# Kernel tuning notes

Measured on AMD Instinct MI355X. Metric: run time of the kernel, lower is better.

Reference implementation:

```python
import jax, jax.numpy as jnp
import numpy as np

H, NH, NKV, HD, S, B = 4096, 32, 8, 128, 2048, 1
QMAX = 127.0  # int8 symmetric


def fake_quant(x, axis=None):
    """Symmetric int8 fake quantization with straight-through estimator.
    axis=None -> per-tensor dynamic scale; axis=int -> per-channel along that axis."""
    if axis is None:
        amax = jnp.max(jnp.abs(x))
    else:
        amax = jnp.max(jnp.abs(x), axis=axis, keepdims=True)
    scale = jnp.maximum(amax, 1e-8) / QMAX
    q = jnp.clip(jnp.round(x / scale), -QMAX - 1, QMAX) * scale
    return x + jax.lax.stop_gradient(q - x)


def quant_linear(x, w):
    # weight: per-output-channel quant (reduce over in-features axis=1);
    # activation: per-tensor dynamic quant
    xq = fake_quant(x)
    wq = fake_quant(w, axis=1)
    return jnp.einsum('bsh,oh->bso', xq, wq)


def rotate_half(x):
    x1, x2 = jnp.split(x, 2, axis=-1)
    return jnp.concatenate([-x2, x1], axis=-1)


def apply_rope(q, k, cos, sin):
    # q: [B,NH,S,HD], k: [B,NKV,S,HD], cos/sin: [B,S,HD]
    cos = cos[:, None, :, :]
    sin = sin[:, None, :, :]
    return q * cos + rotate_half(q) * sin, k * cos + rotate_half(k) * sin


def setup_inputs() -> dict:
    key = jax.random.key(0)
    ks = jax.random.split(key, 6)
    hidden_states = jax.random.normal(ks[0], (B, S, H), jnp.float32)
    # additive causal mask
    neg = jnp.finfo(jnp.float32).min
    mask = jnp.where(jnp.tril(jnp.ones((S, S), bool)), 0.0, neg)
    attention_mask = jnp.broadcast_to(mask, (B, 1, S, S)).astype(jnp.float32)
    # rotary cos/sin
    inv_freq = 1.0 / (10000.0 ** (jnp.arange(0, HD, 2, dtype=jnp.float32) / HD))
    t = jnp.arange(S, dtype=jnp.float32)
    freqs = jnp.outer(t, inv_freq)                     # [S, HD/2]
    emb = jnp.concatenate([freqs, freqs], axis=-1)     # [S, HD]
    cos = jnp.broadcast_to(jnp.cos(emb), (B, S, HD))
    sin = jnp.broadcast_to(jnp.sin(emb), (B, S, HD))
    sc = 0.02
    wq = jax.random.normal(ks[1], (H, H), jnp.float32) * sc
    wk = jax.random.normal(ks[2], (NKV * HD, H), jnp.float32) * sc
    wv = jax.random.normal(ks[3], (NKV * HD, H), jnp.float32) * sc
    wo = jax.random.normal(ks[4], (H, H), jnp.float32) * sc
    return {"hidden_states": hidden_states, "attention_mask": attention_mask,
            "cos": cos, "sin": sin, "wq": wq, "wk": wk, "wv": wv, "wo": wo}


def reference(hidden_states, attention_mask, cos, sin, wq, wk, wv, wo):
    b, s, _ = hidden_states.shape
    scaling = HD ** -0.5
    q = quant_linear(hidden_states, wq).reshape(b, s, NH, HD).transpose(0, 2, 1, 3)
    k = quant_linear(hidden_states, wk).reshape(b, s, NKV, HD).transpose(0, 2, 1, 3)
    v = quant_linear(hidden_states, wv).reshape(b, s, NKV, HD).transpose(0, 2, 1, 3)
    q, k = apply_rope(q, k, cos, sin)
    groups = NH // NKV
    k = jnp.repeat(k, groups, axis=1)  # [B,NH,S,HD]
    v = jnp.repeat(v, groups, axis=1)
    # quantize before QK^T
    qq = fake_quant(q)
    kq = fake_quant(k)
    attn = jnp.einsum('bhqd,bhkd->bhqk', qq, kq) * scaling
    attn = attn + attention_mask
    attn = jnp.maximum(attn, jnp.finfo(attn.dtype).min)
    attn = jax.nn.softmax(attn.astype(jnp.float32), axis=-1).astype(q.dtype)
    # quantize before PV
    pq = fake_quant(attn)
    vq = fake_quant(v)
    out = jnp.einsum('bhqk,bhkd->bhqd', pq, vq)
    out = out.transpose(0, 2, 1, 3).reshape(b, s, NH * HD)
    out = quant_linear(out, wo)
    return out
```

## Files before the change

### kernel.cpp

```cpp
#include <hip/hip_runtime.h>
#include <cstdint>
#include <cstddef>


#define S_LEN   2048
#define HDIM    4096
#define NHEADS  32
#define NKVH    8
#define HEADD   128
#define QMAXF   127.0f
#define ROPE_BLOCKS 20480

typedef _Float16 half8  __attribute__((ext_vector_type(8)));
typedef float    floatx4 __attribute__((ext_vector_type(4)));

__device__ __forceinline__ float wave_max64(float v){
#pragma unroll
  for (int off = 32; off > 0; off >>= 1) v = fmaxf(v, __shfl_xor(v, off));
  return v;
}
__device__ __forceinline__ float grp16_max(float v){
#pragma unroll
  for (int off = 8; off > 0; off >>= 1) v = fmaxf(v, __shfl_xor(v, off));
  return v;
}
__device__ __forceinline__ float grp16_sum(float v){
#pragma unroll
  for (int off = 8; off > 0; off >>= 1) v += __shfl_xor(v, off);
  return v;
}
__device__ __forceinline__ void atomic_max_f(unsigned* p, float v){
  atomicMax(p, __float_as_uint(v));
}
__device__ __forceinline__ float q8(float x, float scale){
  return fminf(fmaxf(rintf(x / scale), -128.f), 127.f);
}
__device__ __forceinline__ void gload_lds16(const _Float16* g, _Float16* l){
  __builtin_amdgcn_global_load_lds((const __attribute__((address_space(1))) void*)g,
                                   (__attribute__((address_space(3))) void*)l, 16, 0, 0);
}

__device__ __forceinline__ void block_atomic_max(float m, unsigned* out){
  m = wave_max64(m);
  __shared__ float red[4];
  int wid = threadIdx.x >> 6;
  if ((threadIdx.x & 63) == 0) red[wid] = m;
  __syncthreads();
  if (threadIdx.x == 0)
    atomic_max_f(out, fmaxf(fmaxf(red[0], red[1]), fmaxf(red[2], red[3])));
}

__global__ void k_init(float* scal){ if (threadIdx.x < 16) scal[threadIdx.x] = 0.0f; }

__global__ void k_amax(const float* __restrict__ x, size_t n4, unsigned* __restrict__ out){
  size_t i = (size_t)blockIdx.x * blockDim.x + threadIdx.x;
  size_t stride = (size_t)gridDim.x * blockDim.x;
  float m = 0.f;
  for (; i < n4; i += stride){
    float4 v = ((const float4*)x)[i];
    m = fmaxf(m, fmaxf(fmaxf(fabsf(v.x), fabsf(v.y)), fmaxf(fabsf(v.z), fabsf(v.w))));
  }
  block_atomic_max(m, out);
}

__global__ void k_amax_v(const float* __restrict__ Y, unsigned* __restrict__ out){
  size_t i = (size_t)blockIdx.x * blockDim.x + threadIdx.x;
  size_t stride = (size_t)gridDim.x * blockDim.x;
  float m = 0.f;
  for (size_t e = i; e < (size_t)S_LEN * 1024; e += stride){
    size_t s = e >> 10; int c = (int)(e & 1023);
    m = fmaxf(m, fabsf(Y[s * 6144 + 5120 + c]));
  }
  block_atomic_max(m, out);
}

__global__ void k_quant(const float* __restrict__ x, _Float16* __restrict__ q,
                        size_t n4, const float* __restrict__ amax){
  float scale = fmaxf(*amax, 1e-8f) / QMAXF;
  size_t i = (size_t)blockIdx.x * blockDim.x + threadIdx.x;
  size_t stride = (size_t)gridDim.x * blockDim.x;
  for (; i < n4; i += stride){
    float4 v = ((const float4*)x)[i];
    union { _Float16 h[4]; uint2 u; } pk;
    pk.h[0] = (_Float16)q8(v.x, scale);
    pk.h[1] = (_Float16)q8(v.y, scale);
    pk.h[2] = (_Float16)q8(v.z, scale);
    pk.h[3] = (_Float16)q8(v.w, scale);
    ((uint2*)q)[i] = pk.u;
  }
}

__global__ __launch_bounds__(256) void k_quant_w(
    const float* __restrict__ wq, const float* __restrict__ wk,
    const float* __restrict__ wv, const float* __restrict__ wo,
    _Float16* __restrict__ Wall, _Float16* __restrict__ Wo,
    float* __restrict__ wsc)
{
  int row = blockIdx.x;
  const float* src; _Float16* dst;
  if (row < 4096)      { src = wq + (size_t)row * HDIM;          dst = Wall + (size_t)row * HDIM; }
  else if (row < 5120) { src = wk + (size_t)(row - 4096) * HDIM; dst = Wall + (size_t)row * HDIM; }
  else if (row < 6144) { src = wv + (size_t)(row - 5120) * HDIM; dst = Wall + (size_t)row * HDIM; }
  else                 { src = wo + (size_t)(row - 6144) * HDIM; dst = Wo + (size_t)(row - 6144) * HDIM; }
  float4 v[4]; float m = 0.f;
#pragma unroll
  for (int i = 0; i < 4; i++){
    v[i] = ((const float4*)src)[threadIdx.x + i * 256];
    m = fmaxf(m, fmaxf(fmaxf(fabsf(v[i].x), fabsf(v[i].y)), fmaxf(fabsf(v[i].z), fabsf(v[i].w))));
  }
  m = wave_max64(m);
  __shared__ float red[4];
  int wid = threadIdx.x >> 6;
  if ((threadIdx.x & 63) == 0) red[wid] = m;
  __syncthreads();
  float am = fmaxf(fmaxf(red[0], red[1]), fmaxf(red[2], red[3]));
  float scale = fmaxf(am, 1e-8f) / QMAXF;
  if (threadIdx.x == 0) wsc[row] = scale;
#pragma unroll
  for (int i = 0; i < 4; i++){
    union { _Float16 h[4]; uint2 u; } pk;
    pk.h[0] = (_Float16)q8(v[i].x, scale);
    pk.h[1] = (_Float16)q8(v[i].y, scale);
    pk.h[2] = (_Float16)q8(v[i].z, scale);
    pk.h[3] = (_Float16)q8(v[i].w, scale);
    ((uint2*)dst)[threadIdx.x + i * 256] = pk.u;
  }
}

__global__ __launch_bounds__(256) void k_rope(
    float* __restrict__ Y, const float* __restrict__ cosb,
    const float* __restrict__ sinb,
    float* __restrict__ qpart, float* __restrict__ kpart)
{
  int idx = blockIdx.x * 256 + threadIdx.x;
  int s = idx / (40 * 64);
  int rem = idx - s * 40 * 64;
  int head = rem >> 6;
  int d = rem & 63;
  size_t base = (size_t)s * 6144 + (head < 32 ? head * 128 : 4096 + (head - 32) * 128);
  float x1 = Y[base + d], x2 = Y[base + d + 64];
  float c1 = cosb[s * 128 + d],      s1 = sinb[s * 128 + d];
  float c2 = cosb[s * 128 + d + 64], s2 = sinb[s * 128 + d + 64];
  float o1 = x1 * c1 - x2 * s1;
  float o2 = x2 * c2 + x1 * s2;
  Y[base + d] = o1; Y[base + d + 64] = o2;
  float m = wave_max64(fmaxf(fabsf(o1), fabsf(o2)));
  __shared__ float wmax[4]; __shared__ int wisq[4];
  int wid = threadIdx.x >> 6;
  if ((threadIdx.x & 63) == 0){ wmax[wid] = m; wisq[wid] = (head < 32); }
  __syncthreads();
  if (threadIdx.x == 0){
    float qm = 0.f, km = 0.f;
#pragma unroll
    for (int w = 0; w < 4; w++){
      if (wisq[w]) qm = fmaxf(qm, wmax[w]); else km = fmaxf(km, wmax[w]);
    }
    qpart[blockIdx.x] = qm; kpart[blockIdx.x] = km;
  }
}

__global__ __launch_bounds__(256) void k_reduce_qk(
    const float* __restrict__ qpart, const float* __restrict__ kpart,
    float* __restrict__ scal)
{
  const float* src = blockIdx.x ? kpart : qpart;
  float m = 0.f;
  for (int i = threadIdx.x; i < ROPE_BLOCKS; i += 256) m = fmaxf(m, src[i]);
  m = wave_max64(m);
  __shared__ float red[4];
  int wid = threadIdx.x >> 6;
  if ((threadIdx.x & 63) == 0) red[wid] = m;
  __syncthreads();
  if (threadIdx.x == 0)
    scal[1 + blockIdx.x] = fmaxf(fmaxf(red[0], red[1]), fmaxf(red[2], red[3]));
}

__global__ __launch_bounds__(256) void k_quant_qk(
    const float* __restrict__ Y, _Float16* __restrict__ Qh,
    _Float16* __restrict__ Kh, const float* __restrict__ scal)
{
  int i = blockIdx.x * 256 + threadIdx.x;
  int s = i / 1280, c4 = i - s * 1280;
  int col = c4 * 4;
  float4 v = *(const float4*)(Y + (size_t)s * 6144 + col);
  float scale = fmaxf(col < 4096 ? scal[1] : scal[2], 1e-8f) / QMAXF;
  union { _Float16 h[4]; uint2 u; } pk;
  pk.h[0] = (_Float16)q8(v.x, scale);
  pk.h[1] = (_Float16)q8(v.y, scale);
  pk.h[2] = (_Float16)q8(v.z, scale);
  pk.h[3] = (_Float16)q8(v.w, scale);
  if (col < 4096) *(uint2*)(Qh + (size_t)s * 4096 + col) = pk.u;
  else            *(uint2*)(Kh + (size_t)s * 1024 + (col - 4096)) = pk.u;
}

__global__ __launch_bounds__(256) void k_quant_vt(
    const float* __restrict__ Y, _Float16* __restrict__ Vt,
    const float* __restrict__ scal)
{
  __shared__ _Float16 sT[64][72];
  const int s0 = blockIdx.x * 64, kvh = blockIdx.y, dh = blockIdx.z;
  const float scale = fmaxf(scal[3], 1e-8f) / QMAXF;
  const int d = threadIdx.x & 63, srow = threadIdx.x >> 6;
#pragma unroll
  for (int i = 0; i < 16; i++){
    int s = srow + i * 4;
    float v = Y[(size_t)(s0 + s) * 6144 + 5120 + kvh * 128 + dh * 64 + d];
    sT[d][s] = (_Float16)q8(v, scale);
  }
  __syncthreads();
  const int dr = threadIdx.x >> 2, j = threadIdx.x & 3;
  _Float16* dst = Vt + (size_t)kvh * HEADD * S_LEN + (size_t)(dh * 64 + dr) * S_LEN + s0 + j * 16;
  *(uint4*)(dst)     = *(const uint4*)(&sT[dr][j * 16]);
  *(uint4*)(dst + 8) = *(const uint4*)(&sT[dr][j * 16 + 8]);
}

__global__ __launch_bounds__(256) void k_gemm_nt(
    const _Float16* __restrict__ A, const _Float16* __restrict__ B,
    const float* __restrict__ amax_a, const float* __restrict__ sb,
    float* __restrict__ C, int M, int N, int K)
{
  __shared__ _Float16 sA[128 * 32];
  __shared__ _Float16 sB[128 * 32];
  const int m0 = blockIdx.x * 128;
  const int n0 = blockIdx.y * 128;
  const int tid = threadIdx.x;
  const int w = tid >> 6, lane = tid & 63;
  const int quad = lane >> 4, l16 = lane & 15;
  const int wm = (w & 1) * 64, wn = (w >> 1) * 64;
  floatx4 acc[4][4] = {};
  const int srow = w * 16 + (lane >> 2);
  const int scol = (lane & 3) * 8;
  const _Float16* gA0 = A + (size_t)(m0 + srow) * K + scol;
  const _Float16* gA1 = A + (size_t)(m0 + 64 + srow) * K + scol;
  const _Float16* gB0 = B + (size_t)(n0 + srow) * K + scol;
  const _Float16* gB1 = B + (size_t)(n0 + 64 + srow) * K + scol;
  _Float16* dA0 = sA + w * 512 + lane * 8;
  _Float16* dA1 = sA + 2048 + w * 512 + lane * 8;
  _Float16* dB0 = sB + w * 512 + lane * 8;
  _Float16* dB1 = sB + 2048 + w * 512 + lane * 8;

  for (int k0 = 0; k0 < K; k0 += 32){
    __syncthreads();
    gload_lds16(gA0 + k0, dA0);
    gload_lds16(gA1 + k0, dA1);
    gload_lds16(gB0 + k0, dB0);
    gload_lds16(gB1 + k0, dB1);
    __syncthreads();
    half8 af[4], bf[4];
#pragma unroll
    for (int i = 0; i < 4; i++){
      af[i] = *(const half8*)(sA + (wm + i * 16 + l16) * 32 + quad * 8);
      bf[i] = *(const half8*)(sB + (wn + i * 16 + l16) * 32 + quad * 8);
    }
#pragma unroll
    for (int i = 0; i < 4; i++)
#pragma unroll
      for (int j = 0; j < 4; j++)
        acc[i][j] = __builtin_amdgcn_mfma_f32_16x16x32_f16(af[i], bf[j], acc[i][j], 0, 0, 0);
  }
  const float sa = fmaxf(*amax_a, 1e-8f) / QMAXF;
#pragma unroll
  for (int i = 0; i < 4; i++){
    int row = m0 + wm + i * 16 + quad * 4;
#pragma unroll
    for (int j = 0; j < 4; j++){
      int col = n0 + wn + j * 16 + l16;
      float sc2 = sa * sb[col];
#pragma unroll
      for (int rr = 0; rr < 4; rr++)
        C[(size_t)(row + rr) * N + col] = acc[i][j][rr] * sc2;
    }
  }
}

__global__ __launch_bounds__(256) void k_attn(
    const _Float16* __restrict__ Qh,
    const _Float16* __restrict__ Kh,
    const _Float16* __restrict__ Vt,
    const float* __restrict__ scal,
    float* __restrict__ AO)
{
  const int h   = blockIdx.y;
  const int kvh = h >> 2;
  const int tid = threadIdx.x;
  const int wid = tid >> 6, lane = tid & 63;
  const int quad = lane >> 4, l16 = lane & 15;

  __shared__ _Float16 sK[64 * 136];
  __shared__ _Float16 sV[128 * 72];
  __shared__ _Float16 sP[4][16 * 72];

  const float s_q = fmaxf(scal[1], 1e-8f) / QMAXF;
  const float s_k = fmaxf(scal[2], 1e-8f) / QMAXF;
  const float s_v = fmaxf(scal[3], 1e-8f) / QMAXF;
  const float qkscale = s_q * s_k * 0.08838834764831845f;
  const float osc = s_v * (1.0f / QMAXF);

  for (int half = 0; half < 2; half++){
    const int qb = half ? (31 - blockIdx.x) : blockIdx.x;
    const int qrow = qb * 64 + wid * 16 + l16;
    half8 qf[4];
#pragma unroll
    for (int kk = 0; kk < 4; kk++)
      qf[kk] = *(const half8*)(Qh + (size_t)qrow * 4096 + h * 128 + kk * 32 + quad * 8);
    const int q_of_reg = qb * 64 + wid * 16 + quad * 4;

    float mrow[4] = { -__builtin_inff(), -__builtin_inff(), -__builtin_inff(), -__builtin_inff() };
    float lrow[4] = { 0.f, 0.f, 0.f, 0.f };

    for (int kt = 0; kt <= qb; ++kt){
      int r = tid >> 2, seg = tid & 3;
      const uint4* gK = (const uint4*)(Kh + (size_t)(kt * 64 + r) * 1024 + kvh * 128 + seg * 32);
      uint4 t0 = gK[0], t1 = gK[1], t2 = gK[2], t3 = gK[3];
      __syncthreads();
      { uint4* d1 = (uint4*)(sK + r * 136 + seg * 32); d1[0] = t0; d1[1] = t1; d1[2] = t2; d1[3] = t3; }
      __syncthreads();
      float sv[4][4];
      const bool diag = (kt == qb);
#pragma unroll
      for (int nt = 0; nt < 4; nt++){
        floatx4 c = {};
#pragma unroll
        for (int kk = 0; kk < 4; kk++){
          half8 bf = *(const half8*)(sK + (nt * 16 + l16) * 136 + kk * 32 + quad * 8);
          c = __builtin_amdgcn_mfma_f32_16x16x32_f16(qf[kk], bf, c, 0, 0, 0);
        }
        if (diag){
          int kpos = kt * 64 + nt * 16 + l16;
#pragma unroll
          for (int rr = 0; rr < 4; rr++)
            sv[nt][rr] = (kpos <= q_of_reg + rr) ? c[rr] * qkscale : -__builtin_inff();
        } else {
#pragma unroll
          for (int rr = 0; rr < 4; rr++) sv[nt][rr] = c[rr] * qkscale;
        }
      }
#pragma unroll
      for (int rr = 0; rr < 4; rr++){
        float lmax = fmaxf(fmaxf(sv[0][rr], sv[1][rr]), fmaxf(sv[2][rr], sv[3][rr]));
        float tmax = grp16_max(lmax);
        float mnew = fmaxf(mrow[rr], tmax);
        float lsum = 0.f;
#pragma unroll
        for (int nt = 0; nt < 4; nt++) lsum += __expf(sv[nt][rr] - mnew);
        lsum = grp16_sum(lsum);
        lrow[rr] = lrow[rr] * __expf(mrow[rr] - mnew) + lsum;
        mrow[rr] = mnew;
      }
    }

    float il[4];
#pragma unroll
    for (int rr = 0; rr < 4; rr++) il[rr] = QMAXF * __builtin_amdgcn_rcpf(lrow[rr]);

    floatx4 accO[8] = {};
    for (int kt = 0; kt <= qb; ++kt){
      int r = tid >> 2, seg = tid & 3;
      const uint4* gK = (const uint4*)(Kh + (size_t)(kt * 64 + r) * 1024 + kvh * 128 + seg * 32);
      uint4 t0 = gK[0], t1 = gK[1], t2 = gK[2], t3 = gK[3];
      int vr = tid >> 1, vh = tid & 1;
      const uint4* gV = (const uint4*)(Vt + (size_t)kvh * HEADD * S_LEN + (size_t)vr * S_LEN + kt * 64 + vh * 32);
      uint4 u0 = gV[0], u1 = gV[1], u2 = gV[2], u3 = gV[3];
      __syncthreads();
      { uint4* d1 = (uint4*)(sK + r * 136 + seg * 32); d1[0] = t0; d1[1] = t1; d1[2] = t2; d1[3] = t3; }
      { uint4* d2 = (uint4*)(sV + vr * 72 + vh * 32);  d2[0] = u0; d2[1] = u1; d2[2] = u2; d2[3] = u3; }
      __syncthreads();
      const bool diag = (kt == qb);
#pragma unroll
      for (int nt = 0; nt < 4; nt++){
        floatx4 c = {};
#pragma unroll
        for (int kk = 0; kk < 4; kk++){
          half8 bf = *(const half8*)(sK + (nt * 16 + l16) * 136 + kk * 32 + quad * 8);
          c = __builtin_amdgcn_mfma_f32_16x16x32_f16(qf[kk], bf, c, 0, 0, 0);
        }
        int kpos = kt * 64 + nt * 16 + l16;
#pragma unroll
        for (int rr = 0; rr < 4; rr++){
          float pq = fminf(rintf(__expf(c[rr] * qkscale - mrow[rr]) * il[rr]), 127.f);
          if (diag && kpos > q_of_reg + rr) pq = 0.f;
          sP[wid][(quad * 4 + rr) * 72 + nt * 16 + l16] = (_Float16)pq;
        }
      }
      __syncthreads();
      half8 pf0 = *(const half8*)(&sP[wid][l16 * 72 + quad * 8]);
      half8 pf1 = *(const half8*)(&sP[wid][l16 * 72 + 32 + quad * 8]);
#pragma unroll
      for (int dt = 0; dt < 8; dt++){
        half8 b0 = *(const half8*)(sV + (dt * 16 + l16) * 72 + quad * 8);
        half8 b1 = *(const half8*)(sV + (dt * 16 + l16) * 72 + 32 + quad * 8);
        accO[dt] = __builtin_amdgcn_mfma_f32_16x16x32_f16(pf0, b0, accO[dt], 0, 0, 0);
        accO[dt] = __builtin_amdgcn_mfma_f32_16x16x32_f16(pf1, b1, accO[dt], 0, 0, 0);
      }
    }

#pragma unroll
    for (int dt = 0; dt < 8; dt++){
      int col = h * 128 + dt * 16 + l16;
#pragma unroll
      for (int rr = 0; rr < 4; rr++)
        AO[(size_t)(q_of_reg + rr) * 4096 + col] = accO[dt][rr] * osc;
    }
  }
}

extern "C" void kernel_launch(void* const* d_in, const int* in_sizes, int n_in,
                              void* d_out, int out_size, void* d_ws, size_t ws_size,
                              hipStream_t stream)
{
  const float* hidden = (const float*)d_in[0];
  const float* cosb = (const float*)d_in[2];
  const float* sinb = (const float*)d_in[3];
  const float* wq = (const float*)d_in[4];
  const float* wk = (const float*)d_in[5];
  const float* wv = (const float*)d_in[6];
  const float* wo = (const float*)d_in[7];
  float* out = (float*)d_out;

  char* ws = (char*)d_ws;
  size_t off = 0;
  auto alloc = [&](size_t bytes){ size_t o = off; off += (bytes + 255) & ~(size_t)255; return o; };
  float*    scal  = (float*)   (ws + alloc(64));
  float*    wsc   = (float*)   (ws + alloc(10240 * 4));
  float*    qpart = (float*)   (ws + alloc(ROPE_BLOCKS * 4));
  float*    kpart = (float*)   (ws + alloc(ROPE_BLOCKS * 4));
  _Float16* Wall  = (_Float16*)(ws + alloc((size_t)6144 * 4096 * 2));
  _Float16* Wo    = (_Float16*)(ws + alloc((size_t)4096 * 4096 * 2));
  _Float16* Xq    = (_Float16*)(ws + alloc((size_t)2048 * 4096 * 2));
  float*    Y     = (float*)   (ws + alloc((size_t)2048 * 6144 * 4));
  _Float16* Qh  = Xq;
  _Float16* Kh  = Wall;
  _Float16* Vt  = Wall + (size_t)2048 * 1024;
  float*    AO  = Y;
  _Float16* AOq = (_Float16*)((char*)Y + (size_t)2048 * 4096 * 4);

  unsigned* su = (unsigned*)scal;

  k_init<<<dim3(1), dim3(64), 0, stream>>>(scal);
  k_quant_w<<<dim3(10240), dim3(256), 0, stream>>>(wq, wk, wv, wo, Wall, Wo, wsc);
  k_amax<<<dim3(256), dim3(256), 0, stream>>>(hidden, (size_t)(2048 * 4096 / 4), su + 0);
  k_quant<<<dim3(2048), dim3(256), 0, stream>>>(hidden, Xq, (size_t)(2048 * 4096 / 4), scal + 0);
  k_gemm_nt<<<dim3(16, 48), dim3(256), 0, stream>>>(Xq, Wall, scal + 0, wsc, Y, 2048, 6144, 4096);
  k_rope<<<dim3(ROPE_BLOCKS), dim3(256), 0, stream>>>(Y, cosb, sinb, qpart, kpart);
  k_reduce_qk<<<dim3(2), dim3(256), 0, stream>>>(qpart, kpart, scal);
  k_amax_v<<<dim3(256), dim3(256), 0, stream>>>(Y, su + 3);
  k_quant_qk<<<dim3(10240), dim3(256), 0, stream>>>(Y, Qh, Kh, scal);
  k_quant_vt<<<dim3(32, 8, 2), dim3(256), 0, stream>>>(Y, Vt, scal);
  k_attn<<<dim3(16, 32), dim3(256), 0, stream>>>(Qh, Kh, Vt, scal, AO);
  k_amax<<<dim3(256), dim3(256), 0, stream>>>(AO, (size_t)(2048 * 4096 / 4), su + 4);
  k_quant<<<dim3(2048), dim3(256), 0, stream>>>(AO, AOq, (size_t)(2048 * 4096 / 4), scal + 4);
  k_gemm_nt<<<dim3(16, 32), dim3(256), 0, stream>>>(AOq, Wo, scal + 4, wsc + 6144, out, 2048, 4096, 4096);
}
```

Measured before the change: 683.2 us.

## Restructure attention kernel: one q-block per CTA, double-buffered K prefetch, swizzled LDS

The attention kernel now assigns one query block per workgroup (grid doubled to 32x32) instead of pairing two causal halves. It spreads block order across head groups for load balance. It double-buffers K tiles in the first softmax-statistics pass and prefetches K/V into registers for the next iteration in the second pass. Padded shared-memory layouts are replaced with XOR-swizzled layouts, and setprio hints and launch_bounds(256,4) are added. The goal is to hide global-load latency, cut bank conflicts and raise occupancy, at the cost of more register pressure and the loss of the paired-block balancing.

Measured after the change: 735.5 us. 7.7% more time.

```diff
diff --git a/kernel.cpp b/kernel.cpp
--- a/kernel.cpp
+++ b/kernel.cpp
@@ -273,22 +273,24 @@
   }
 }
 
-__global__ __launch_bounds__(256) void k_attn(
+__global__ __launch_bounds__(256, 4) void k_attn(
     const _Float16* __restrict__ Qh,
     const _Float16* __restrict__ Kh,
     const _Float16* __restrict__ Vt,
     const float* __restrict__ scal,
     float* __restrict__ AO)
 {
+  const int jj = blockIdx.y >> 3;
+  const int aa = (jj & 2) ? (int)((blockIdx.x + 16) & 31) : (int)blockIdx.x;
+  const int qb = (jj & 1) ? (31 - aa) : aa;
   const int h   = blockIdx.y;
   const int kvh = h >> 2;
   const int tid = threadIdx.x;
   const int wid = tid >> 6, lane = tid & 63;
   const int quad = lane >> 4, l16 = lane & 15;
 
-  __shared__ _Float16 sK[64 * 136];
-  __shared__ _Float16 sV[128 * 72];
-  __shared__ _Float16 sP[4][16 * 72];
+  __shared__ _Float16 sKV[2][8192];
+  __shared__ _Float16 sP[4][1024];
 
   const float s_q = fmaxf(scal[1], 1e-8f) / QMAXF;
   const float s_k = fmaxf(scal[2], 1e-8f) / QMAXF;
@@ -296,111 +298,169 @@
   const float qkscale = s_q * s_k * 0.08838834764831845f;
   const float osc = s_v * (1.0f / QMAXF);
 
-  for (int half = 0; half < 2; half++){
-    const int qb = half ? (31 - blockIdx.x) : blockIdx.x;
-    const int qrow = qb * 64 + wid * 16 + l16;
-    half8 qf[4];
-#pragma unroll
-    for (int kk = 0; kk < 4; kk++)
-      qf[kk] = *(const half8*)(Qh + (size_t)qrow * 4096 + h * 128 + kk * 32 + quad * 8);
-    const int q_of_reg = qb * 64 + wid * 16 + quad * 4;
-
-    float mrow[4] = { -__builtin_inff(), -__builtin_inff(), -__builtin_inff(), -__builtin_inff() };
-    float lrow[4] = { 0.f, 0.f, 0.f, 0.f };
-
-    for (int kt = 0; kt <= qb; ++kt){
-      int r = tid >> 2, seg = tid & 3;
-      const uint4* gK = (const uint4*)(Kh + (size_t)(kt * 64 + r) * 1024 + kvh * 128 + seg * 32);
-      uint4 t0 = gK[0], t1 = gK[1], t2 = gK[2], t3 = gK[3];
-      __syncthreads();
-      { uint4* d1 = (uint4*)(sK + r * 136 + seg * 32); d1[0] = t0; d1[1] = t1; d1[2] = t2; d1[3] = t3; }
-      __syncthreads();
-      float sv[4][4];
-      const bool diag = (kt == qb);
-#pragma unroll
-      for (int nt = 0; nt < 4; nt++){
-        floatx4 c = {};
-#pragma unroll
-        for (int kk = 0; kk < 4; kk++){
-          half8 bf = *(const half8*)(sK + (nt * 16 + l16) * 136 + kk * 32 + quad * 8);
-          c = __builtin_amdgcn_mfma_f32_16x16x32_f16(qf[kk], bf, c, 0, 0, 0);
-        }
-        if (diag){
-          int kpos = kt * 64 + nt * 16 + l16;
-#pragma unroll
-          for (int rr = 0; rr < 4; rr++)
-            sv[nt][rr] = (kpos <= q_of_reg + rr) ? c[rr] * qkscale : -__builtin_inff();
-        } else {
-#pragma unroll
-          for (int rr = 0; rr < 4; rr++) sv[nt][rr] = c[rr] * qkscale;
-        }
+  const int r   = tid >> 2, seg = tid & 3;
+  int kst[4];
+#pragma unroll
+  for (int i = 0; i < 4; i++){
+    int c = seg * 4 + i;
+    kst[i] = r * 128 + ((c & 8) | ((c ^ (r & 7)) & 7)) * 8;
+  }
+  const int vr = tid >> 1, vh = tid & 1;
+  int vst[4];
+#pragma unroll
+  for (int i = 0; i < 4; i++){
+    int c = vh * 4 + i;
+    vst[i] = vr * 64 + ((c ^ (vr & 7)) & 7) * 8;
+  }
+  int krd[4];
+#pragma unroll
+  for (int kk = 0; kk < 4; kk++){
+    int c = kk * 4 + quad;
+    krd[kk] = l16 * 128 + ((c & 8) | ((c ^ (l16 & 7)) & 7)) * 8;
+  }
+  const int vrd0 = l16 * 64 + ((quad       ^ (l16 & 7)) & 7) * 8;
+  const int vrd1 = l16 * 64 + (((quad ^ 4) ^ (l16 & 7)) & 7) * 8;
+
+  const _Float16* gK0 = Kh + (size_t)r * 1024 + (size_t)kvh * 128 + seg * 32;
+  const _Float16* gV0 = Vt + (size_t)kvh * (HEADD * S_LEN) + (size_t)vr * S_LEN + vh * 32;
+
+  const int qrow = qb * 64 + wid * 16 + l16;
+  half8 qf[4];
+#pragma unroll
+  for (int kk = 0; kk < 4; kk++)
+    qf[kk] = *(const half8*)(Qh + (size_t)qrow * 4096 + h * 128 + kk * 32 + quad * 8);
+  const int q_of_reg = qb * 64 + wid * 16 + quad * 4;
+
+  float mrow[4], lrow[4];
+#pragma unroll
+  for (int rr = 0; rr < 4; rr++){ mrow[rr] = -__builtin_inff(); lrow[rr] = 0.f; }
+
+  {
+    const uint4* g = (const uint4*)gK0;
+    uint4 t0 = g[0], t1 = g[1], t2 = g[2], t3 = g[3];
+    _Float16* b = sKV[0];
+    *(uint4*)(b + kst[0]) = t0; *(uint4*)(b + kst[1]) = t1;
+    *(uint4*)(b + kst[2]) = t2; *(uint4*)(b + kst[3]) = t3;
+  }
+  __syncthreads();
+
+  for (int kt = 0; kt <= qb; ++kt){
+    uint4 t0, t1, t2, t3;
+    if (kt < qb){
+      const uint4* g = (const uint4*)(gK0 + (size_t)(kt + 1) * 65536);
+      t0 = g[0]; t1 = g[1]; t2 = g[2]; t3 = g[3];
+    }
+    const _Float16* kb = sKV[kt & 1];
+    float sv[4][4];
+    const bool diag = (kt == qb);
+    __builtin_amdgcn_s_setprio(1);
+#pragma unroll
+    for (int nt = 0; nt < 4; nt++){
+      floatx4 c = {};
+#pragma unroll
+      for (int kk = 0; kk < 4; kk++){
+        half8 bf = *(const half8*)(kb + nt * 2048 + krd[kk]);
+        c = __builtin_amdgcn_mfma_f32_16x16x32_f16(qf[kk], bf, c, 0, 0, 0);
       }
+      if (diag){
+        int kpos = kt * 64 + nt * 16 + l16;
+#pragma unroll
+        for (int rr = 0; rr < 4; rr++)
+          sv[nt][rr] = (kpos <= q_of_reg + rr) ? c[rr] * qkscale : -__builtin_inff();
+      } else {
+#pragma unroll
+        for (int rr = 0; rr < 4; rr++) sv[nt][rr] = c[rr] * qkscale;
+      }
+    }
+    __builtin_amdgcn_s_setprio(0);
+    if (kt < qb){
+      _Float16* b = sKV[(kt + 1) & 1];
+      *(uint4*)(b + kst[0]) = t0; *(uint4*)(b + kst[1]) = t1;
+      *(uint4*)(b + kst[2]) = t2; *(uint4*)(b + kst[3]) = t3;
+    }
+#pragma unroll
+    for (int rr = 0; rr < 4; rr++){
+      float lmax = fmaxf(fmaxf(sv[0][rr], sv[1][rr]), fmaxf(sv[2][rr], sv[3][rr]));
+      float tmax = grp16_max(lmax);
+      float mnew = fmaxf(mrow[rr], tmax);
+      float lsum = 0.f;
+#pragma unroll
+      for (int nt = 0; nt < 4; nt++) lsum += __expf(sv[nt][rr] - mnew);
+      lsum = grp16_sum(lsum);
+      lrow[rr] = lrow[rr] * __expf(mrow[rr] - mnew) + lsum;
+      mrow[rr] = mnew;
+    }
+    __syncthreads();
+  }
+
+  float il[4];
+#pragma unroll
+  for (int rr = 0; rr < 4; rr++) il[rr] = QMAXF * __builtin_amdgcn_rcpf(lrow[rr]);
+
+  floatx4 accO[8] = {};
+  _Float16* sKb = sKV[0];
+  _Float16* sVb = sKV[1];
+  _Float16* sPw = sP[wid];
+
+  uint4 t0, t1, t2, t3, u0, u1, u2, u3;
+  {
+    const uint4* g  = (const uint4*)gK0;
+    t0 = g[0];  t1 = g[1];  t2 = g[2];  t3 = g[3];
+    const uint4* gv = (const uint4*)gV0;
+    u0 = gv[0]; u1 = gv[1]; u2 = gv[2]; u3 = gv[3];
+  }
+  for (int kt = 0; kt <= qb; ++kt){
+    __syncthreads();
+    *(uint4*)(sKb + kst[0]) = t0; *(uint4*)(sKb + kst[1]) = t1;
+    *(uint4*)(sKb + kst[2]) = t2; *(uint4*)(sKb + kst[3]) = t3;
+    *(uint4*)(sVb + vst[0]) = u0; *(uint4*)(sVb + vst[1]) = u1;
+    *(uint4*)(sVb + vst[2]) = u2; *(uint4*)(sVb + vst[3]) = u3;
+    __syncthreads();
+    const bool diag = (kt == qb);
+    __builtin_amdgcn_s_setprio(1);
+#pragma unroll
+    for (int nt = 0; nt < 4; nt++){
+      floatx4 c = {};
+#pragma unroll
+      for (int kk = 0; kk < 4; kk++){
+        half8 bf = *(const half8*)(sKb + nt * 2048 + krd[kk]);
+        c = __builtin_amdgcn_mfma_f32_16x16x32_f16(qf[kk], bf, c, 0, 0, 0);
+      }
+      int kpos = kt * 64 + nt * 16 + l16;
 #pragma unroll
       for (int rr = 0; rr < 4; rr++){
-        float lmax = fmaxf(fmaxf(sv[0][rr], sv[1][rr]), fmaxf(sv[2][rr], sv[3][rr]));
-        float tmax = grp16_max(lmax);
-        float mnew = fmaxf(mrow[rr], tmax);
-        float lsum = 0.f;
-#pragma unroll
-        for (int nt = 0; nt < 4; nt++) lsum += __expf(sv[nt][rr] - mnew);
-        lsum = grp16_sum(lsum);
-        lrow[rr] = lrow[rr] * __expf(mrow[rr] - mnew) + lsum;
-        mrow[rr] = mnew;
+        float pq = fminf(rintf(__expf(c[rr] * qkscale - mrow[rr]) * il[rr]), 127.f);
+        if (diag && kpos > q_of_reg + rr) pq = 0.f;
+        int row = quad * 4 + rr;
+        sPw[row * 64 + ((nt * 2 + (l16 >> 3)) ^ (row & 7)) * 8 + (l16 & 7)] = (_Float16)pq;
       }
     }
-
-    float il[4];
-#pragma unroll
-    for (int rr = 0; rr < 4; rr++) il[rr] = QMAXF * __builtin_amdgcn_rcpf(lrow[rr]);
-
-    floatx4 accO[8] = {};
-    for (int kt = 0; kt <= qb; ++kt){
-      int r = tid >> 2, seg = tid & 3;
-      const uint4* gK = (const uint4*)(Kh + (size_t)(kt * 64 + r) * 1024 + kvh * 128 + seg * 32);
-      uint4 t0 = gK[0], t1 = gK[1], t2 = gK[2], t3 = gK[3];
-      int vr = tid >> 1, vh = tid & 1;
-      const uint4* gV = (const uint4*)(Vt + (size_t)kvh * HEADD * S_LEN + (size_t)vr * S_LEN + kt * 64 + vh * 32);
-      uint4 u0 = gV[0], u1 = gV[1], u2 = gV[2], u3 = gV[3];
-      __syncthreads();
-      { uint4* d1 = (uint4*)(sK + r * 136 + seg * 32); d1[0] = t0; d1[1] = t1; d1[2] = t2; d1[3] = t3; }
-      { uint4* d2 = (uint4*)(sV + vr * 72 + vh * 32);  d2[0] = u0; d2[1] = u1; d2[2] = u2; d2[3] = u3; }
-      __syncthreads();
-      const bool diag = (kt == qb);
-#pragma unroll
-      for (int nt = 0; nt < 4; nt++){
-        floatx4 c = {};
-#pragma unroll
-        for (int kk = 0; kk < 4; kk++){
-          half8 bf = *(const half8*)(sK + (nt * 16 + l16) * 136 + kk * 32 + quad * 8);
-          c = __builtin_amdgcn_mfma_f32_16x16x32_f16(qf[kk], bf, c, 0, 0, 0);
-        }
-        int kpos = kt * 64 + nt * 16 + l16;
-#pragma unroll
-        for (int rr = 0; rr < 4; rr++){
-          float pq = fminf(rintf(__expf(c[rr] * qkscale - mrow[rr]) * il[rr]), 127.f);
-          if (diag && kpos > q_of_reg + rr) pq = 0.f;
-          sP[wid][(quad * 4 + rr) * 72 + nt * 16 + l16] = (_Float16)pq;
-        }
-      }
-      __syncthreads();
-      half8 pf0 = *(const half8*)(&sP[wid][l16 * 72 + quad * 8]);
-      half8 pf1 = *(const half8*)(&sP[wid][l16 * 72 + 32 + quad * 8]);
-#pragma unroll
-      for (int dt = 0; dt < 8; dt++){
-        half8 b0 = *(const half8*)(sV + (dt * 16 + l16) * 72 + quad * 8);
-        half8 b1 = *(const half8*)(sV + (dt * 16 + l16) * 72 + 32 + quad * 8);
-        accO[dt] = __builtin_amdgcn_mfma_f32_16x16x32_f16(pf0, b0, accO[dt], 0, 0, 0);
-        accO[dt] = __builtin_amdgcn_mfma_f32_16x16x32_f16(pf1, b1, accO[dt], 0, 0, 0);
-      }
-    }
-
+    __builtin_amdgcn_s_setprio(0);
+    if (kt < qb){
+      const uint4* g  = (const uint4*)(gK0 + (size_t)(kt + 1) * 65536);
+      t0 = g[0];  t1 = g[1];  t2 = g[2];  t3 = g[3];
+      const uint4* gv = (const uint4*)(gV0 + (size_t)(kt + 1) * 64);
+      u0 = gv[0]; u1 = gv[1]; u2 = gv[2]; u3 = gv[3];
+    }
+    half8 pf0 = *(const half8*)(sPw + vrd0);
+    half8 pf1 = *(const half8*)(sPw + vrd1);
+    __builtin_amdgcn_s_setprio(1);
 #pragma unroll
     for (int dt = 0; dt < 8; dt++){
-      int col = h * 128 + dt * 16 + l16;
-#pragma unroll
-      for (int rr = 0; rr < 4; rr++)
-        AO[(size_t)(q_of_reg + rr) * 4096 + col] = accO[dt][rr] * osc;
-    }
+      half8 b0 = *(const half8*)(sVb + dt * 1024 + vrd0);
+      half8 b1 = *(const half8*)(sVb + dt * 1024 + vrd1);
+      accO[dt] = __builtin_amdgcn_mfma_f32_16x16x32_f16(pf0, b0, accO[dt], 0, 0, 0);
+      accO[dt] = __builtin_amdgcn_mfma_f32_16x16x32_f16(pf1, b1, accO[dt], 0, 0, 0);
+    }
+    __builtin_amdgcn_s_setprio(0);
+  }
+
+#pragma unroll
+  for (int dt = 0; dt < 8; dt++){
+    int col = h * 128 + dt * 16 + l16;
+#pragma unroll
+    for (int rr = 0; rr < 4; rr++)
+      AO[(size_t)(q_of_reg + rr) * 4096 + col] = accO[dt][rr] * osc;
   }
 }
 
@@ -446,7 +506,7 @@
   k_amax_v<<<dim3(256), dim3(256), 0, stream>>>(Y, su + 3);
   k_quant_qk<<<dim3(10240), dim3(256), 0, stream>>>(Y, Qh, Kh, scal);
   k_quant_vt<<<dim3(32, 8, 2), dim3(256), 0, stream>>>(Y, Vt, scal);
-  k_attn<<<dim3(16, 32), dim3(256), 0, stream>>>(Qh, Kh, Vt, scal, AO);
+  k_attn<<<dim3(32, 32), dim3(256), 0, stream>>>(Qh, Kh, Vt, scal, AO);
   k_amax<<<dim3(256), dim3(256), 0, stream>>>(AO, (size_t)(2048 * 4096 / 4), su + 4);
   k_quant<<<dim3(2048), dim3(256), 0, stream>>>(AO, AOq, (size_t)(2048 * 4096 / 4), scal + 4);
   k_gemm_nt<<<dim3(16, 32), dim3(256), 0, stream>>>(AOq, Wo, scal + 4, wsc + 6144, out, 2048, 4096, 4096);
```
